# Optimization experiments

Hardware: AMD Instinct MI355X
Metric: run time of the kernel (lower is better)

## Reference

```python
import jax, jax.numpy as jnp
import numpy as np

NUM_RANGES = 31   # bins [0,1)...[29,30) plus [30, inf) -> max_height=30
EPS = 1e-06
ALPHA = 0.5
NAN_VALUE = -1.0


def setup_inputs() -> dict:
    key = jax.random.key(0)
    k1, k2 = jax.random.split(key)
    shape = (64, 512, 512)
    # targets in log1p space; natural heights expm1(target) span [0, ~34)
    target = jax.random.uniform(k1, shape, dtype=jnp.float32) * 3.55
    pred = target + 0.1 * jax.random.normal(k2, shape, dtype=jnp.float32)
    return {"pred": pred, "target": target}


def reference(pred, target):
    valid = target != NAN_VALUE                      # no-data mask
    natural = jnp.expm1(target)                      # heights in natural space
    # arithmetic bin index: ranges [i, i+1) for i<30, last bin [30, inf)
    bin_idx = jnp.clip(jnp.floor(natural), 0.0, NUM_RANGES - 1).astype(jnp.int32)
    in_range = natural >= 0.0                        # samples below 0 fall in no range

    # histogram of valid, in-range samples (scatter-add)
    counts = jnp.zeros(NUM_RANGES, jnp.float32).at[bin_idx.ravel()].add(
        (valid & in_range).ravel().astype(jnp.float32))
    total_valid = jnp.sum(valid).astype(jnp.float32)
    denom = jnp.maximum(total_valid, 1.0)
    freq = counts / denom
    w = 1.0 / (freq ** ALPHA + EPS)                  # inverse-frequency weights, [31]

    base = jnp.abs(pred - target)                    # L1 in log1p space
    sample_w = jnp.where(in_range, w[bin_idx], 0.0)  # gather per-sample weight
    weighted = base * sample_w
    # mean over valid samples (out-of-range valid samples contribute 0, as in torch)
    mean_loss = jnp.sum(jnp.where(valid, weighted, 0.0)) / denom
    return mean_loss
```

## Files before the change

### kernel.cpp

```cpp
#include <hip/hip_runtime.h>
#include <math.h>

#define NBINS 31
#define NSLOT 32
#define NCOPIES 256
#define BLOCK 256
#define GRID 1024

#define CNT_SHIFT 25
#define SUM_MASK  0x1FFFFFFu
#define FIX_SCALE 32768.0f


__device__ __forceinline__ void prep(float p, float t, unsigned hbase,
                                     unsigned& addr, unsigned& pk, unsigned& nvalid)
{
    nvalid += (t != -1.0f) ? 1u : 0u;
    bool ok = (t >= 0.0f);
    float nat = __expf(t) - 1.0f;
    unsigned b = (unsigned)(int)fminf(nat, 30.0f);
    unsigned pkv = (1u << CNT_SHIFT)
                 | (unsigned)(fabsf(p - t) * FIX_SCALE + 0.5f);
    pk   = ok ? pkv : 0u;
    addr = hbase + ((ok ? b : 31u) << 10);
}

__device__ __forceinline__ void packet(float4 p, float4 t, unsigned hbase,
                                       unsigned& nvalid)
{
    unsigned a0, a1, a2, a3, k0, k1, k2, k3;
    prep(p.x, t.x, hbase, a0, k0, nvalid);
    prep(p.y, t.y, hbase, a1, k1, nvalid);
    prep(p.z, t.z, hbase, a2, k2, nvalid);
    prep(p.w, t.w, hbase, a3, k3, nvalid);

    unsigned r0, r1, r2, r3;
    asm volatile(
        "ds_read_b32 %0, %4\n\t"
        "ds_read_b32 %1, %5\n\t"
        "ds_read_b32 %2, %6\n\t"
        "ds_read_b32 %3, %7"
        : "=&v"(r0), "=&v"(r1), "=&v"(r2), "=&v"(r3)
        : "v"(a0), "v"(a1), "v"(a2), "v"(a3));

    unsigned s0 = k0;
    unsigned s1 = k1 + (a1 == a0 ? s0 : 0u);
    unsigned s2 = k2 + (a2 == a1 ? s1 : (a2 == a0 ? s0 : 0u));
    unsigned s3 = k3 + (a3 == a2 ? s2 : (a3 == a1 ? s1 : (a3 == a0 ? s0 : 0u)));

    asm volatile(
        "s_waitcnt lgkmcnt(0)\n\t"
        "v_add_u32 %0, %0, %4\n\t"
        "v_add_u32 %1, %1, %5\n\t"
        "v_add_u32 %2, %2, %6\n\t"
        "v_add_u32 %3, %3, %7\n\t"
        "ds_write_b32 %8, %0\n\t"
        "ds_write_b32 %9, %1\n\t"
        "ds_write_b32 %10, %2\n\t"
        "ds_write_b32 %11, %3"
        : "+v"(r0), "+v"(r1), "+v"(r2), "+v"(r3)
        : "v"(s0), "v"(s1), "v"(s2), "v"(s3),
          "v"(a0), "v"(a1), "v"(a2), "v"(a3)
        : "memory");
}

__global__ __launch_bounds__(BLOCK) void zero_ws_kernel(unsigned* ws)
{
    int t = threadIdx.x;
    if (t < 192) ws[t] = 0u;
}

__global__ __launch_bounds__(BLOCK) void hist_kernel(
    const float* __restrict__ pred, const float* __restrict__ target, int n,
    float* __restrict__ g_sums, unsigned* __restrict__ g_cnts,
    unsigned* __restrict__ g_total)
{
    __shared__ unsigned s_hist[NSLOT * NCOPIES];
    __shared__ float    p_sum[NBINS * 8];
    __shared__ unsigned p_cnt[NBINS * 8];
    __shared__ unsigned s_tot[BLOCK / 64];

    const int tid = threadIdx.x;
    for (int i = tid; i < NSLOT * NCOPIES; i += BLOCK) s_hist[i] = 0u;
    __syncthreads();

    const unsigned hbase = (unsigned)(uintptr_t)(void*)s_hist + ((unsigned)tid << 2);
    unsigned nvalid = 0;

    const int n4 = n >> 2;
    const float4* __restrict__ pred4 = (const float4*)pred;
    const float4* __restrict__ targ4 = (const float4*)target;
    const int st = gridDim.x * BLOCK;
    const int i0 = blockIdx.x * BLOCK + tid;

    if (n4 > 0) {
        float4 pA, tA, pB, tB;
        {
            int ia = (i0      < n4) ? i0      : 0;
            int ib = (i0 + st < n4) ? i0 + st : 0;
            pA = pred4[ia]; tA = targ4[ia];
            pB = pred4[ib]; tB = targ4[ib];
        }
        for (int i = i0; i < n4; i += 2 * st) {
            int ca = (i + 2 * st < n4) ? i + 2 * st : 0;
            int cb = (i + 3 * st < n4) ? i + 3 * st : 0;
            float4 pNA = pred4[ca], tNA = targ4[ca];
            packet(pA, tA, hbase, nvalid);
            float4 pNB = pred4[cb], tNB = targ4[cb];
            if (i + st < n4) packet(pB, tB, hbase, nvalid);
            pA = pNA; tA = tNA; pB = pNB; tB = tNB;
        }
    }
    for (int i = (n4 << 2) + i0; i < n; i += st) {
        float p = pred[i], t = target[i];
        nvalid += (t != -1.0f) ? 1u : 0u;
        if (t >= 0.0f) {
            float nat = __expf(t) - 1.0f;
            int b = (int)fminf(nat, 30.0f);
            s_hist[b * NCOPIES + tid] += (1u << CNT_SHIFT)
                | (unsigned)(fabsf(p - t) * FIX_SCALE + 0.5f);
        }
    }
    asm volatile("s_waitcnt lgkmcnt(0)" ::: "memory");
    __syncthreads();

    if (tid < NBINS * 8) {
        const int b = tid >> 3, g = tid & 7;
        const uint4* row = (const uint4*)(s_hist + b * NCOPIES);
        float fs = 0.0f; unsigned cs = 0u;
        #pragma unroll
        for (int kk = 0; kk < 8; ++kk) {
            uint4 v = row[g + 8 * kk];
            cs += (v.x >> CNT_SHIFT) + (v.y >> CNT_SHIFT)
                + (v.z >> CNT_SHIFT) + (v.w >> CNT_SHIFT);
            fs += (float)(v.x & SUM_MASK) + (float)(v.y & SUM_MASK)
                + (float)(v.z & SUM_MASK) + (float)(v.w & SUM_MASK);
        }
        p_sum[tid] = fs;
        p_cnt[tid] = cs;
    }
    unsigned v = nvalid;
    #pragma unroll
    for (int off = 32; off >= 1; off >>= 1) v += __shfl_down(v, off, 64);
    if ((tid & 63) == 0) s_tot[tid >> 6] = v;
    __syncthreads();

    if (tid < NBINS) {
        float fs = 0.0f; unsigned cs = 0u;
        #pragma unroll
        for (int g = 0; g < 8; ++g) { fs += p_sum[tid * 8 + g]; cs += p_cnt[tid * 8 + g]; }
        atomicAdd(&g_sums[tid], fs * (1.0f / FIX_SCALE));
        atomicAdd(&g_cnts[tid], cs);
    }
    if (tid == 0) {
        unsigned tot = 0;
        #pragma unroll
        for (int w = 0; w < BLOCK / 64; ++w) tot += s_tot[w];
        atomicAdd(g_total, tot);
    }
}

__global__ void finalize_kernel(const float* __restrict__ g_sums,
                                const unsigned* __restrict__ g_cnts,
                                const unsigned* __restrict__ g_total,
                                float* __restrict__ out)
{
    int lane = threadIdx.x;
    float denom = fmaxf((float)(*g_total), 1.0f);
    float contrib = 0.0f;
    if (lane < NBINS) {
        float freq = (float)g_cnts[lane] / denom;
        float w = 1.0f / (sqrtf(freq) + 1e-6f);
        contrib = g_sums[lane] * w;
    }
    #pragma unroll
    for (int off = 32; off >= 1; off >>= 1) contrib += __shfl_down(contrib, off, 64);
    if (lane == 0) *out = contrib / denom;
}

extern "C" void kernel_launch(void* const* d_in, const int* in_sizes, int n_in,
                              void* d_out, int out_size, void* d_ws, size_t ws_size,
                              hipStream_t stream)
{
    const float* pred   = (const float*)d_in[0];
    const float* target = (const float*)d_in[1];
    float* out = (float*)d_out;
    int n = in_sizes[0];

    float*    g_sums  = (float*)d_ws;
    unsigned* g_cnts  = (unsigned*)d_ws + 64;
    unsigned* g_total = (unsigned*)d_ws + 128;

    zero_ws_kernel<<<1, BLOCK, 0, stream>>>((unsigned*)d_ws);

    hist_kernel<<<GRID, BLOCK, 0, stream>>>(pred, target, n, g_sums, g_cnts, g_total);

    finalize_kernel<<<1, 64, 0, stream>>>(g_sums, g_cnts, g_total, out);
}
```

Baseline: 149.6 us.

## Deepen load pipeline, count valid with ballot, fuse finalize via last-block ticket

```diff
diff --git a/kernel.cpp b/kernel.cpp
--- a/kernel.cpp
+++ b/kernel.cpp
@@ -13,12 +13,11 @@
 
 
 __device__ __forceinline__ void prep(float p, float t, unsigned hbase,
-                                     unsigned& addr, unsigned& pk, unsigned& nvalid)
-{
-    nvalid += (t != -1.0f) ? 1u : 0u;
+                                     unsigned& addr, unsigned& pk)
+{
     bool ok = (t >= 0.0f);
     float nat = __expf(t) - 1.0f;
-    unsigned b = (unsigned)(int)fminf(nat, 30.0f);
+    unsigned b = (unsigned)fminf(nat, 30.0f);
     unsigned pkv = (1u << CNT_SHIFT)
                  | (unsigned)(fabsf(p - t) * FIX_SCALE + 0.5f);
     pk   = ok ? pkv : 0u;
@@ -26,13 +25,18 @@
 }
 
 __device__ __forceinline__ void packet(float4 p, float4 t, unsigned hbase,
-                                       unsigned& nvalid)
-{
+                                       unsigned& wcnt)
+{
+    wcnt += (unsigned)__popcll(__ballot(t.x != -1.0f));
+    wcnt += (unsigned)__popcll(__ballot(t.y != -1.0f));
+    wcnt += (unsigned)__popcll(__ballot(t.z != -1.0f));
+    wcnt += (unsigned)__popcll(__ballot(t.w != -1.0f));
+
     unsigned a0, a1, a2, a3, k0, k1, k2, k3;
-    prep(p.x, t.x, hbase, a0, k0, nvalid);
-    prep(p.y, t.y, hbase, a1, k1, nvalid);
-    prep(p.z, t.z, hbase, a2, k2, nvalid);
-    prep(p.w, t.w, hbase, a3, k3, nvalid);
+    prep(p.x, t.x, hbase, a0, k0);
+    prep(p.y, t.y, hbase, a1, k1);
+    prep(p.z, t.z, hbase, a2, k2);
+    prep(p.w, t.w, hbase, a3, k3);
 
     unsigned r0, r1, r2, r3;
     asm volatile(
@@ -70,22 +74,25 @@
     if (t < 192) ws[t] = 0u;
 }
 
-__global__ __launch_bounds__(BLOCK) void hist_kernel(
+__global__ __launch_bounds__(BLOCK, 4) void hist_kernel(
     const float* __restrict__ pred, const float* __restrict__ target, int n,
     float* __restrict__ g_sums, unsigned* __restrict__ g_cnts,
-    unsigned* __restrict__ g_total)
+    unsigned* __restrict__ g_total, unsigned* __restrict__ g_ticket,
+    float* __restrict__ out)
 {
     __shared__ unsigned s_hist[NSLOT * NCOPIES];
     __shared__ float    p_sum[NBINS * 8];
     __shared__ unsigned p_cnt[NBINS * 8];
     __shared__ unsigned s_tot[BLOCK / 64];
+    __shared__ unsigned s_last;
 
     const int tid = threadIdx.x;
     for (int i = tid; i < NSLOT * NCOPIES; i += BLOCK) s_hist[i] = 0u;
     __syncthreads();
 
     const unsigned hbase = (unsigned)(uintptr_t)(void*)s_hist + ((unsigned)tid << 2);
-    unsigned nvalid = 0;
+    unsigned wcnt = 0;
+    unsigned tcnt = 0;
 
     const int n4 = n >> 2;
     const float4* __restrict__ pred4 = (const float4*)pred;
@@ -93,27 +100,34 @@
     const int st = gridDim.x * BLOCK;
     const int i0 = blockIdx.x * BLOCK + tid;
 
-    if (n4 > 0) {
-        float4 pA, tA, pB, tB;
-        {
-            int ia = (i0      < n4) ? i0      : 0;
-            int ib = (i0 + st < n4) ? i0 + st : 0;
-            pA = pred4[ia]; tA = targ4[ia];
-            pB = pred4[ib]; tB = targ4[ib];
-        }
-        for (int i = i0; i < n4; i += 2 * st) {
-            int ca = (i + 2 * st < n4) ? i + 2 * st : 0;
-            int cb = (i + 3 * st < n4) ? i + 3 * st : 0;
-            float4 pNA = pred4[ca], tNA = targ4[ca];
-            packet(pA, tA, hbase, nvalid);
-            float4 pNB = pred4[cb], tNB = targ4[cb];
-            if (i + st < n4) packet(pB, tB, hbase, nvalid);
-            pA = pNA; tA = tNA; pB = pNB; tB = tNB;
-        }
-    }
+#define LOADC(P, T, idx)                                   \
+    do { int c_ = (idx); c_ = (c_ < n4) ? c_ : 0;          \
+         P = pred4[c_]; T = targ4[c_]; } while (0)
+
+    if (i0 < n4) {
+        float4 P0, T0, P1, T1, P2, T2, P3, T3;
+        LOADC(P0, T0, i0);
+        LOADC(P1, T1, i0 + st);
+        LOADC(P2, T2, i0 + 2 * st);
+        LOADC(P3, T3, i0 + 3 * st);
+        for (int i = i0; i < n4; i += 4 * st) {
+            float4 a0, b0, a1, b1, a2, b2, a3, b3;
+            LOADC(a0, b0, i + 4 * st);
+            LOADC(a1, b1, i + 5 * st);
+            LOADC(a2, b2, i + 6 * st);
+            LOADC(a3, b3, i + 7 * st);
+            packet(P0, T0, hbase, wcnt);
+            if (i +     st < n4) packet(P1, T1, hbase, wcnt);
+            if (i + 2 * st < n4) packet(P2, T2, hbase, wcnt);
+            if (i + 3 * st < n4) packet(P3, T3, hbase, wcnt);
+            P0 = a0; T0 = b0; P1 = a1; T1 = b1;
+            P2 = a2; T2 = b2; P3 = a3; T3 = b3;
+        }
+    }
+#undef LOADC
     for (int i = (n4 << 2) + i0; i < n; i += st) {
         float p = pred[i], t = target[i];
-        nvalid += (t != -1.0f) ? 1u : 0u;
+        tcnt += (t != -1.0f) ? 1u : 0u;
         if (t >= 0.0f) {
             float nat = __expf(t) - 1.0f;
             int b = (int)fminf(nat, 30.0f);
@@ -139,10 +153,10 @@
         p_sum[tid] = fs;
         p_cnt[tid] = cs;
     }
-    unsigned v = nvalid;
+    unsigned v = tcnt;
     #pragma unroll
     for (int off = 32; off >= 1; off >>= 1) v += __shfl_down(v, off, 64);
-    if ((tid & 63) == 0) s_tot[tid >> 6] = v;
+    if ((tid & 63) == 0) s_tot[tid >> 6] = wcnt + v;
     __syncthreads();
 
     if (tid < NBINS) {
@@ -158,24 +172,27 @@
         for (int w = 0; w < BLOCK / 64; ++w) tot += s_tot[w];
         atomicAdd(g_total, tot);
     }
-}
-
-__global__ void finalize_kernel(const float* __restrict__ g_sums,
-                                const unsigned* __restrict__ g_cnts,
-                                const unsigned* __restrict__ g_total,
-                                float* __restrict__ out)
-{
-    int lane = threadIdx.x;
-    float denom = fmaxf((float)(*g_total), 1.0f);
-    float contrib = 0.0f;
-    if (lane < NBINS) {
-        float freq = (float)g_cnts[lane] / denom;
-        float w = 1.0f / (sqrtf(freq) + 1e-6f);
-        contrib = g_sums[lane] * w;
-    }
-    #pragma unroll
-    for (int off = 32; off >= 1; off >>= 1) contrib += __shfl_down(contrib, off, 64);
-    if (lane == 0) *out = contrib / denom;
+
+    __threadfence();
+    __syncthreads();
+    if (tid == 0)
+        s_last = (atomicAdd(g_ticket, 1u) == (unsigned)gridDim.x - 1u) ? 1u : 0u;
+    __syncthreads();
+    if (s_last && tid < 64) {
+        __threadfence();
+        int lane = tid;
+        float denom = fmaxf((float)atomicAdd(g_total, 0u), 1.0f);
+        float contrib = 0.0f;
+        if (lane < NBINS) {
+            float fs = atomicAdd(&g_sums[lane], 0.0f);
+            float freq = (float)atomicAdd(&g_cnts[lane], 0u) / denom;
+            float w = 1.0f / (sqrtf(freq) + 1e-6f);
+            contrib = fs * w;
+        }
+        #pragma unroll
+        for (int off = 32; off >= 1; off >>= 1) contrib += __shfl_down(contrib, off, 64);
+        if (lane == 0) *out = contrib / denom;
+    }
 }
 
 extern "C" void kernel_launch(void* const* d_in, const int* in_sizes, int n_in,
@@ -187,13 +204,13 @@
     float* out = (float*)d_out;
     int n = in_sizes[0];
 
-    float*    g_sums  = (float*)d_ws;
-    unsigned* g_cnts  = (unsigned*)d_ws + 64;
-    unsigned* g_total = (unsigned*)d_ws + 128;
+    float*    g_sums   = (float*)d_ws;
+    unsigned* g_cnts   = (unsigned*)d_ws + 64;
+    unsigned* g_total  = (unsigned*)d_ws + 128;
+    unsigned* g_ticket = (unsigned*)d_ws + 129;
 
     zero_ws_kernel<<<1, BLOCK, 0, stream>>>((unsigned*)d_ws);
 
-    hist_kernel<<<GRID, BLOCK, 0, stream>>>(pred, target, n, g_sums, g_cnts, g_total);
-
-    finalize_kernel<<<1, 64, 0, stream>>>(g_sums, g_cnts, g_total, out);
-}
+    hist_kernel<<<GRID, BLOCK, 0, stream>>>(pred, target, n, g_sums, g_cnts,
+                                            g_total, g_ticket, out);
+}
```

Measured after the change: 283.4 us. +89.4%, slower.

## Fuse finalize into histogram kernel via last-block ticket and specialize the even-trip loop

Applied to the files above, without the earlier changes.

```diff
diff --git a/kernel.cpp b/kernel.cpp
--- a/kernel.cpp
+++ b/kernel.cpp
@@ -60,8 +60,7 @@
         "ds_write_b32 %11, %3"
         : "+v"(r0), "+v"(r1), "+v"(r2), "+v"(r3)
         : "v"(s0), "v"(s1), "v"(s2), "v"(s3),
-          "v"(a0), "v"(a1), "v"(a2), "v"(a3)
-        : "memory");
+          "v"(a0), "v"(a1), "v"(a2), "v"(a3));
 }
 
 __global__ __launch_bounds__(BLOCK) void zero_ws_kernel(unsigned* ws)
@@ -70,18 +69,25 @@
     if (t < 192) ws[t] = 0u;
 }
 
-__global__ __launch_bounds__(BLOCK) void hist_kernel(
+__global__ __launch_bounds__(BLOCK, 4) void hist_kernel(
     const float* __restrict__ pred, const float* __restrict__ target, int n,
     float* __restrict__ g_sums, unsigned* __restrict__ g_cnts,
-    unsigned* __restrict__ g_total)
+    unsigned* __restrict__ g_total, unsigned* __restrict__ g_ticket,
+    float* __restrict__ out)
 {
     __shared__ unsigned s_hist[NSLOT * NCOPIES];
     __shared__ float    p_sum[NBINS * 8];
     __shared__ unsigned p_cnt[NBINS * 8];
     __shared__ unsigned s_tot[BLOCK / 64];
+    __shared__ unsigned s_last;
 
     const int tid = threadIdx.x;
-    for (int i = tid; i < NSLOT * NCOPIES; i += BLOCK) s_hist[i] = 0u;
+    {
+        uint4 z = make_uint4(0u, 0u, 0u, 0u);
+        uint4* h4 = (uint4*)s_hist;
+        #pragma unroll
+        for (int k = 0; k < (NSLOT * NCOPIES / 4) / BLOCK; ++k) h4[tid + k * BLOCK] = z;
+    }
     __syncthreads();
 
     const unsigned hbase = (unsigned)(uintptr_t)(void*)s_hist + ((unsigned)tid << 2);
@@ -92,33 +98,38 @@
     const float4* __restrict__ targ4 = (const float4*)target;
     const int st = gridDim.x * BLOCK;
     const int i0 = blockIdx.x * BLOCK + tid;
-
-    if (n4 > 0) {
-        float4 pA, tA, pB, tB;
-        {
-            int ia = (i0      < n4) ? i0      : 0;
-            int ib = (i0 + st < n4) ? i0 + st : 0;
-            pA = pred4[ia]; tA = targ4[ia];
-            pB = pred4[ib]; tB = targ4[ib];
-        }
-        for (int i = i0; i < n4; i += 2 * st) {
-            int ca = (i + 2 * st < n4) ? i + 2 * st : 0;
-            int cb = (i + 3 * st < n4) ? i + 3 * st : 0;
-            float4 pNA = pred4[ca], tNA = targ4[ca];
+    const int T  = n4 / st;
+
+    if ((n4 % st) == 0 && (n & 3) == 0 && T >= 2 && (T & 1) == 0) {
+        float4 pA = pred4[i0],      tA = targ4[i0];
+        float4 pB = pred4[i0 + st], tB = targ4[i0 + st];
+        int i = i0 + 2 * st;
+        for (int k = 0; k < T - 2; k += 2, i += 2 * st) {
+            float4 pNA = pred4[i],      tNA = targ4[i];
+            float4 pNB = pred4[i + st], tNB = targ4[i + st];
             packet(pA, tA, hbase, nvalid);
-            float4 pNB = pred4[cb], tNB = targ4[cb];
-            if (i + st < n4) packet(pB, tB, hbase, nvalid);
+            packet(pB, tB, hbase, nvalid);
             pA = pNA; tA = tNA; pB = pNB; tB = tNB;
         }
-    }
-    for (int i = (n4 << 2) + i0; i < n; i += st) {
-        float p = pred[i], t = target[i];
-        nvalid += (t != -1.0f) ? 1u : 0u;
-        if (t >= 0.0f) {
-            float nat = __expf(t) - 1.0f;
-            int b = (int)fminf(nat, 30.0f);
-            s_hist[b * NCOPIES + tid] += (1u << CNT_SHIFT)
-                | (unsigned)(fabsf(p - t) * FIX_SCALE + 0.5f);
+        packet(pA, tA, hbase, nvalid);
+        packet(pB, tB, hbase, nvalid);
+    } else {
+        for (int i = i0; i < n4; i += st) {
+            float4 p = pred4[i];
+            float4 t = targ4[i];
+            packet(p, t, hbase, nvalid);
+        }
+        for (int i = (n4 << 2) + i0; i < n; i += st) {
+            float p = pred[i], t = target[i];
+            if (t != -1.0f) {
+                atomicAdd(g_total, 1u);
+                if (t >= 0.0f) {
+                    float nat = __expf(t) - 1.0f;
+                    int b = (int)fminf(nat, 30.0f);
+                    atomicAdd(&g_sums[b], fabsf(p - t));
+                    atomicAdd(&g_cnts[b], 1u);
+                }
+            }
         }
     }
     asm volatile("s_waitcnt lgkmcnt(0)" ::: "memory");
@@ -158,24 +169,27 @@
         for (int w = 0; w < BLOCK / 64; ++w) tot += s_tot[w];
         atomicAdd(g_total, tot);
     }
-}
-
-__global__ void finalize_kernel(const float* __restrict__ g_sums,
-                                const unsigned* __restrict__ g_cnts,
-                                const unsigned* __restrict__ g_total,
-                                float* __restrict__ out)
-{
-    int lane = threadIdx.x;
-    float denom = fmaxf((float)(*g_total), 1.0f);
-    float contrib = 0.0f;
-    if (lane < NBINS) {
-        float freq = (float)g_cnts[lane] / denom;
-        float w = 1.0f / (sqrtf(freq) + 1e-6f);
-        contrib = g_sums[lane] * w;
-    }
-    #pragma unroll
-    for (int off = 32; off >= 1; off >>= 1) contrib += __shfl_down(contrib, off, 64);
-    if (lane == 0) *out = contrib / denom;
+
+    __threadfence();
+    __syncthreads();
+    if (tid == 0)
+        s_last = (atomicAdd(g_ticket, 1u) == (unsigned)gridDim.x - 1u) ? 1u : 0u;
+    __syncthreads();
+    if (s_last && tid < 64) {
+        __threadfence();
+        int lane = tid;
+        float denom = fmaxf((float)atomicAdd(g_total, 0u), 1.0f);
+        float contrib = 0.0f;
+        if (lane < NBINS) {
+            float fs = atomicAdd(&g_sums[lane], 0.0f);
+            float freq = (float)atomicAdd(&g_cnts[lane], 0u) / denom;
+            float w = 1.0f / (sqrtf(freq) + 1e-6f);
+            contrib = fs * w;
+        }
+        #pragma unroll
+        for (int off = 32; off >= 1; off >>= 1) contrib += __shfl_down(contrib, off, 64);
+        if (lane == 0) *out = contrib / denom;
+    }
 }
 
 extern "C" void kernel_launch(void* const* d_in, const int* in_sizes, int n_in,
@@ -187,13 +201,13 @@
     float* out = (float*)d_out;
     int n = in_sizes[0];
 
-    float*    g_sums  = (float*)d_ws;
-    unsigned* g_cnts  = (unsigned*)d_ws + 64;
-    unsigned* g_total = (unsigned*)d_ws + 128;
+    float*    g_sums   = (float*)d_ws;
+    unsigned* g_cnts   = (unsigned*)d_ws + 64;
+    unsigned* g_total  = (unsigned*)d_ws + 128;
+    unsigned* g_ticket = (unsigned*)d_ws + 129;
 
     zero_ws_kernel<<<1, BLOCK, 0, stream>>>((unsigned*)d_ws);
 
-    hist_kernel<<<GRID, BLOCK, 0, stream>>>(pred, target, n, g_sums, g_cnts, g_total);
-
-    finalize_kernel<<<1, 64, 0, stream>>>(g_sums, g_cnts, g_total, out);
-}
+    hist_kernel<<<GRID, BLOCK, 0, stream>>>(pred, target, n, g_sums, g_cnts,
+                                            g_total, g_ticket, out);
+}
```

Measured after the change: 266.3 us. 78.0% more time.

## Stage global loads directly into LDS with double buffering and shrink grid

Applied to the files above, without the earlier changes.

```diff
diff --git a/kernel.cpp b/kernel.cpp
--- a/kernel.cpp
+++ b/kernel.cpp
@@ -5,11 +5,13 @@
 #define NSLOT 32
 #define NCOPIES 256
 #define BLOCK 256
-#define GRID 1024
+#define GRID 768
 
 #define CNT_SHIFT 25
 #define SUM_MASK  0x1FFFFFFu
 #define FIX_SCALE 32768.0f
+
+typedef float f4 __attribute__((ext_vector_type(4)));
 
 
 __device__ __forceinline__ void prep(float p, float t, unsigned hbase,
@@ -25,7 +27,7 @@
     addr = hbase + ((ok ? b : 31u) << 10);
 }
 
-__device__ __forceinline__ void packet(float4 p, float4 t, unsigned hbase,
+__device__ __forceinline__ void packet(f4 p, f4 t, unsigned hbase,
                                        unsigned& nvalid)
 {
     unsigned a0, a1, a2, a3, k0, k1, k2, k3;
@@ -60,8 +62,28 @@
         "ds_write_b32 %11, %3"
         : "+v"(r0), "+v"(r1), "+v"(r2), "+v"(r3)
         : "v"(s0), "v"(s1), "v"(s2), "v"(s3),
-          "v"(a0), "v"(a1), "v"(a2), "v"(a3)
-        : "memory");
+          "v"(a0), "v"(a1), "v"(a2), "v"(a3));
+}
+
+__device__ __forceinline__ void stage(unsigned* dst, const f4* p4, const f4* t4,
+                                      int idx)
+{
+    __builtin_amdgcn_global_load_lds(
+        (const __attribute__((address_space(1))) unsigned*)(const void*)(p4 + idx),
+        (__attribute__((address_space(3))) unsigned*)dst, 16, 0, 0);
+    __builtin_amdgcn_global_load_lds(
+        (const __attribute__((address_space(1))) unsigned*)(const void*)(t4 + idx),
+        (__attribute__((address_space(3))) unsigned*)(dst + 256), 16, 0, 0);
+}
+
+__device__ __forceinline__ void unstage(unsigned sa, f4& pv, f4& tv)
+{
+    asm volatile(
+        "ds_read_b128 %0, %2\n\t"
+        "ds_read_b128 %1, %2 offset:1024\n\t"
+        "s_waitcnt lgkmcnt(0)"
+        : "=&v"(pv), "=&v"(tv)
+        : "v"(sa));
 }
 
 __global__ __launch_bounds__(BLOCK) void zero_ws_kernel(unsigned* ws)
@@ -70,55 +92,76 @@
     if (t < 192) ws[t] = 0u;
 }
 
-__global__ __launch_bounds__(BLOCK) void hist_kernel(
+__global__ __launch_bounds__(BLOCK, 3) void hist_kernel(
     const float* __restrict__ pred, const float* __restrict__ target, int n,
     float* __restrict__ g_sums, unsigned* __restrict__ g_cnts,
     unsigned* __restrict__ g_total)
 {
     __shared__ unsigned s_hist[NSLOT * NCOPIES];
+    __shared__ unsigned s_stage[2][BLOCK / 64][512];
     __shared__ float    p_sum[NBINS * 8];
     __shared__ unsigned p_cnt[NBINS * 8];
     __shared__ unsigned s_tot[BLOCK / 64];
 
     const int tid = threadIdx.x;
-    for (int i = tid; i < NSLOT * NCOPIES; i += BLOCK) s_hist[i] = 0u;
+    {
+        uint4 z = make_uint4(0u, 0u, 0u, 0u);
+        uint4* h4 = (uint4*)s_hist;
+        #pragma unroll
+        for (int k = 0; k < (NSLOT * NCOPIES / 4) / BLOCK; ++k) h4[tid + k * BLOCK] = z;
+    }
     __syncthreads();
 
     const unsigned hbase = (unsigned)(uintptr_t)(void*)s_hist + ((unsigned)tid << 2);
+    const int lane = tid & 63, wv = tid >> 6;
+    unsigned* stA = &s_stage[0][wv][0];
+    unsigned* stB = &s_stage[1][wv][0];
+    const unsigned saA = (unsigned)(uintptr_t)(void*)stA + ((unsigned)lane << 4);
+    const unsigned saB = (unsigned)(uintptr_t)(void*)stB + ((unsigned)lane << 4);
     unsigned nvalid = 0;
 
     const int n4 = n >> 2;
-    const float4* __restrict__ pred4 = (const float4*)pred;
-    const float4* __restrict__ targ4 = (const float4*)target;
-    const int st = gridDim.x * BLOCK;
+    const f4* __restrict__ pred4 = (const f4*)pred;
+    const f4* __restrict__ targ4 = (const f4*)target;
+    const int st = GRID * BLOCK;
     const int i0 = blockIdx.x * BLOCK + tid;
 
-    if (n4 > 0) {
-        float4 pA, tA, pB, tB;
-        {
-            int ia = (i0      < n4) ? i0      : 0;
-            int ib = (i0 + st < n4) ? i0 + st : 0;
-            pA = pred4[ia]; tA = targ4[ia];
-            pB = pred4[ib]; tB = targ4[ib];
-        }
-        for (int i = i0; i < n4; i += 2 * st) {
-            int ca = (i + 2 * st < n4) ? i + 2 * st : 0;
-            int cb = (i + 3 * st < n4) ? i + 3 * st : 0;
-            float4 pNA = pred4[ca], tNA = targ4[ca];
-            packet(pA, tA, hbase, nvalid);
-            float4 pNB = pred4[cb], tNB = targ4[cb];
-            if (i + st < n4) packet(pB, tB, hbase, nvalid);
-            pA = pNA; tA = tNA; pB = pNB; tB = tNB;
-        }
-    }
-    for (int i = (n4 << 2) + i0; i < n; i += st) {
-        float p = pred[i], t = target[i];
-        nvalid += (t != -1.0f) ? 1u : 0u;
-        if (t >= 0.0f) {
-            float nat = __expf(t) - 1.0f;
-            int b = (int)fminf(nat, 30.0f);
-            s_hist[b * NCOPIES + tid] += (1u << CNT_SHIFT)
-                | (unsigned)(fabsf(p - t) * FIX_SCALE + 0.5f);
+    if ((n & 3) == 0 && (n4 & 63) == 0) {
+        int i = i0;
+        if (i < n4) {
+            stage(stA, pred4, targ4, i);
+            bool curA = true;
+            for (; i + st < n4; i += st) {
+                if (curA) stage(stB, pred4, targ4, i + st);
+                else      stage(stA, pred4, targ4, i + st);
+                asm volatile("s_waitcnt vmcnt(2)" ::: "memory");
+                f4 pv, tv;
+                unstage(curA ? saA : saB, pv, tv);
+                packet(pv, tv, hbase, nvalid);
+                curA = !curA;
+            }
+            asm volatile("s_waitcnt vmcnt(0)" ::: "memory");
+            f4 pv, tv;
+            unstage(curA ? saA : saB, pv, tv);
+            packet(pv, tv, hbase, nvalid);
+        }
+    } else {
+        for (int i = i0; i < n4; i += st) {
+            f4 p = pred4[i];
+            f4 t = targ4[i];
+            packet(p, t, hbase, nvalid);
+        }
+        for (int i = (n4 << 2) + i0; i < n; i += st) {
+            float p = pred[i], t = target[i];
+            if (t != -1.0f) {
+                atomicAdd(g_total, 1u);
+                if (t >= 0.0f) {
+                    float nat = __expf(t) - 1.0f;
+                    int b = (int)fminf(nat, 30.0f);
+                    atomicAdd(&g_sums[b], fabsf(p - t));
+                    atomicAdd(&g_cnts[b], 1u);
+                }
+            }
         }
     }
     asm volatile("s_waitcnt lgkmcnt(0)" ::: "memory");
```

After: 147.7 us. No clear change (-1.3%).
